# Optimization experiments

Hardware: AMD Instinct MI355X
Metric: run time of the kernel (lower is better)

The kernel has to match this reference:

```python
import jax, jax.numpy as jnp
import numpy as np

BS, DIM, HID, T = 4096, 64, 256, 101
GAMMA = 0.1
EPS = 1e-12  # pinverse guard for the 1x1 matrix G G^T


def setup_inputs() -> dict:
    key = jax.random.key(0)
    k0, k1, k2, k3 = jax.random.split(key, 4)
    return {
        "y0": jax.random.normal(k0, (BS, DIM), dtype=jnp.float32),
        "t": jnp.linspace(0.0, 1.0, T).astype(jnp.float32),
        "W1": jax.random.normal(k1, (DIM, HID), dtype=jnp.float32) * 0.05,
        "b1": jnp.zeros((HID,), dtype=jnp.float32),
        "W2": jax.random.normal(k2, (HID, DIM), dtype=jnp.float32) * 0.05,
        "b2": jnp.zeros((DIM,), dtype=jnp.float32),
        "wg": jax.random.normal(k3, (DIM,), dtype=jnp.float32) * 0.1,
        "bg": jnp.zeros((), dtype=jnp.float32),
    }


def reference(y0, t, W1, b1, W2, b2, wg, bg):
    # f_model: 2-layer tanh MLP (ignores t, as is common for autonomous dynamics)
    def f_model(ti, u):
        return jnp.tanh(u @ W1 + b1) @ W2 + b2  # (bs, dim)

    # g_fn: scalar constraint per sample
    def g_single(ui):
        return jnp.tanh(ui @ wg + bg)  # scalar

    def dynamic(ti, u):
        f_u = f_model(ti, u)                              # (bs, dim)
        g_u = jax.vmap(g_single)(u)                       # (bs,)
        # Torch detaches u before autograd Jacobian (create_graph keeps param path)
        G = jax.vmap(jax.grad(g_single))(jax.lax.stop_gradient(u))  # (bs, dim) == G_u row
        # F_u = G^T (G G^T)^+ ; G G^T is 1x1 -> scalar pinverse
        s = jnp.sum(G * G, axis=-1)                       # (bs,)
        pinv = jnp.where(jnp.abs(s) > EPS, 1.0 / s, 0.0)  # (bs,)
        stable = GAMMA * (g_u * pinv)[:, None] * G        # (bs, dim)
        return f_u - stable

    dt = t[1] - t[0]  # Euler solver uses constant dt

    def step(y, ti):
        y_new = y + dynamic(ti, y) * dt
        return y_new, y_new

    _, ys = jax.lax.scan(step, y0, t[:-1])
    return jnp.concatenate([y0[None], ys], axis=0)  # (T, bs, dim)
```

## Files before the change

kernel.cpp:

```cpp
#include <hip/hip_runtime.h>


#define GAMMA 0.1f
#define EPSG  1e-12f

typedef __attribute__((ext_vector_type(8))) short bf16x8;
typedef __attribute__((ext_vector_type(4))) float f32x4;

__device__ __forceinline__ float ftanh(float x) {
    float e = __expf(2.0f * x);
    return 1.0f - 2.0f * __builtin_amdgcn_rcpf(e + 1.0f);
}

__device__ __forceinline__ unsigned int f2bf(float f) {
    unsigned int u = __float_as_uint(f);
    return (u + 0x7fffu + ((u >> 16) & 1u)) >> 16;
}

__global__ __launch_bounds__(512, 1) void snde_kernel(
    const float* __restrict__ y0, const float* __restrict__ t,
    const float* __restrict__ W1, const float* __restrict__ b1,
    const float* __restrict__ W2, const float* __restrict__ b2,
    const float* __restrict__ wg, const float* __restrict__ bgp,
    float* __restrict__ out)
{
    __shared__ unsigned short uAs[16 * 64];
    __shared__ unsigned short hAs[16 * 256];
    __shared__ float          fpart[8][16][68];

    const int tid = threadIdx.x;
    const int w   = tid >> 6;
    const int l   = tid & 63;
    const int l15 = l & 15;
    const int lg  = l >> 4;
    const int s0g = blockIdx.x * 16;

    bf16x8 B1[2][2];
    #pragma unroll
    for (int nt = 0; nt < 2; ++nt) {
        const int n = w * 32 + nt * 16 + l15;
        #pragma unroll
        for (int kt = 0; kt < 2; ++kt) {
            bf16x8 v;
            #pragma unroll
            for (int j = 0; j < 8; ++j) {
                const int k = kt * 32 + lg * 8 + j;
                v[j] = (short)f2bf(W1[k * 256 + n]);
            }
            B1[nt][kt] = v;
        }
    }
    bf16x8 B2[4];
    #pragma unroll
    for (int nt = 0; nt < 4; ++nt) {
        const int n = nt * 16 + l15;
        bf16x8 v;
        #pragma unroll
        for (int j = 0; j < 8; ++j) {
            const int k = w * 32 + lg * 8 + j;
            v[j] = (short)f2bf(W2[k * 64 + n]);
        }
        B2[nt] = v;
    }

    float b1v[2];
    #pragma unroll
    for (int nt = 0; nt < 2; ++nt) b1v[nt] = b1[w * 32 + nt * 16 + l15];

    const int sU = tid >> 5;
    const int dd = (tid & 31) * 2;
    const float2 wg2  = *(const float2*)(&wg[dd]);
    const float2 b2v2 = *(const float2*)(&b2[dd]);
    float wsum = wg2.x * wg2.x + wg2.y * wg2.y;
    #pragma unroll
    for (int m = 1; m < 32; m <<= 1) wsum += __shfl_xor(wsum, m, 64);
    const float bg  = bgp[0];
    const float dtv = t[1] - t[0];

    float2 uv;
    {
        uv = *(const float2*)(&y0[(size_t)(s0g + sU) * 64 + dd]);
        unsigned int p0 = f2bf(uv.x) | (f2bf(uv.y) << 16);
        unsigned int off = (((unsigned)(sU * 128 + dd * 2)) ^ ((unsigned)(sU & 7) << 4)) >> 2;
        ((unsigned int*)uAs)[off] = p0;
        *(float2*)(&out[(size_t)(s0g + sU) * 64 + dd]) = uv;
    }
    __syncthreads();

    for (int step = 0; step < 100; ++step) {
        bf16x8 A1[2];
        #pragma unroll
        for (int kt = 0; kt < 2; ++kt) {
            unsigned int boff = ((unsigned)(l15 * 128 + (kt * 32 + lg * 8) * 2))
                              ^ ((unsigned)(l15 & 7) << 4);
            A1[kt] = *(const bf16x8*)((const char*)uAs + boff);
        }
        f32x4 acc1[2];
        #pragma unroll
        for (int nt = 0; nt < 2; ++nt) {
            acc1[nt][0] = b1v[nt]; acc1[nt][1] = b1v[nt];
            acc1[nt][2] = b1v[nt]; acc1[nt][3] = b1v[nt];
        }
        #pragma unroll
        for (int nt = 0; nt < 2; ++nt)
            #pragma unroll
            for (int kt = 0; kt < 2; ++kt)
                acc1[nt] = __builtin_amdgcn_mfma_f32_16x16x32_bf16(A1[kt], B1[nt][kt], acc1[nt], 0, 0, 0);

        #pragma unroll
        for (int nt = 0; nt < 2; ++nt) {
            const int n = w * 32 + nt * 16 + l15;
            #pragma unroll
            for (int i = 0; i < 4; ++i) {
                const int m = lg * 4 + i;
                const float th = ftanh(acc1[nt][i]);
                unsigned int boff = ((unsigned)(m * 512 + n * 2)) ^ ((unsigned)(m & 7) << 4);
                *(unsigned short*)((char*)hAs + boff) = (unsigned short)f2bf(th);
            }
        }

        bf16x8 A2;
        {
            unsigned int boff = ((unsigned)(l15 * 512 + (w * 32 + lg * 8) * 2))
                              ^ ((unsigned)(l15 & 7) << 4);
            A2 = *(const bf16x8*)((const char*)hAs + boff);
        }
        f32x4 acc2[4];
        #pragma unroll
        for (int nt = 0; nt < 4; ++nt) {
            acc2[nt][0] = 0.f; acc2[nt][1] = 0.f; acc2[nt][2] = 0.f; acc2[nt][3] = 0.f;
        }
        #pragma unroll
        for (int nt = 0; nt < 4; ++nt)
            acc2[nt] = __builtin_amdgcn_mfma_f32_16x16x32_bf16(A2, B2[nt], acc2[nt], 0, 0, 0);

        #pragma unroll
        for (int nt = 0; nt < 4; ++nt) {
            const int n = nt * 16 + l15;
            #pragma unroll
            for (int i = 0; i < 4; ++i)
                fpart[w][lg * 4 + i][n] = acc2[nt][i];
        }
        __syncthreads();

        {
            float2 fs = {0.f, 0.f};
            #pragma unroll
            for (int p = 0; p < 8; ++p) {
                const float2 fp = *(const float2*)(&fpart[p][sU][dd]);
                fs.x += fp.x; fs.y += fp.y;
            }
            float zp = uv.x * wg2.x + uv.y * wg2.y;
            #pragma unroll
            for (int m = 1; m < 32; m <<= 1) zp += __shfl_xor(zp, m, 64);
            const float th = ftanh(zp + bg);
            const float q  = 1.0f - th * th;
            const float sg = q * q * wsum;
            const float pinv = (fabsf(sg) > EPSG) ? __builtin_amdgcn_rcpf(sg) : 0.0f;
            const float coef = GAMMA * th * pinv * q;
            float2 un;
            un.x = uv.x + (fs.x + b2v2.x - coef * wg2.x) * dtv;
            un.y = uv.y + (fs.y + b2v2.y - coef * wg2.y) * dtv;
            uv = un;
            unsigned int p0 = f2bf(un.x) | (f2bf(un.y) << 16);
            unsigned int off = (((unsigned)(sU * 128 + dd * 2)) ^ ((unsigned)(sU & 7) << 4)) >> 2;
            ((unsigned int*)uAs)[off] = p0;
            *(float2*)(&out[(size_t)(step + 1) * (4096 * 64) + (size_t)(s0g + sU) * 64 + dd]) = un;
        }
        __syncthreads();
    }
}

extern "C" void kernel_launch(void* const* d_in, const int* in_sizes, int n_in,
                              void* d_out, int out_size, void* d_ws, size_t ws_size,
                              hipStream_t stream) {
    const float* y0 = (const float*)d_in[0];
    const float* t  = (const float*)d_in[1];
    const float* W1 = (const float*)d_in[2];
    const float* b1 = (const float*)d_in[3];
    const float* W2 = (const float*)d_in[4];
    const float* b2 = (const float*)d_in[5];
    const float* wg = (const float*)d_in[6];
    const float* bg = (const float*)d_in[7];
    float* out = (float*)d_out;

    snde_kernel<<<dim3(256), dim3(512), 0, stream>>>(y0, t, W1, b1, W2, b2, wg, bg, out);
}
```

Before: 111.2 us.

## Halve samples per block to launch 512 blocks and raise occupancy bound

Each block now handles 8 samples instead of 16, and the grid grows from 256 to 512 blocks so every CU on the device gets work. The MFMA tiles stay 16 rows wide with the unused rows zero-filled, so half of the matrix work in each block is padding. Each wave now owns one sample, so the per-sample reduction spans 64 lanes. The launch bound is raised to allow several blocks per CU. This spreads the sequential 100-step loop across more CUs and hides barrier latency, at the cost of wasted MFMA work and scalar instead of float2 stores.

```diff
diff --git a/kernel.cpp b/kernel.cpp
--- a/kernel.cpp
+++ b/kernel.cpp
@@ -17,7 +17,7 @@
     return (u + 0x7fffu + ((u >> 16) & 1u)) >> 16;
 }
 
-__global__ __launch_bounds__(512, 1) void snde_kernel(
+__global__ __launch_bounds__(512, 4) void snde_kernel(
     const float* __restrict__ y0, const float* __restrict__ t,
     const float* __restrict__ W1, const float* __restrict__ b1,
     const float* __restrict__ W2, const float* __restrict__ b2,
@@ -33,7 +33,7 @@
     const int l   = tid & 63;
     const int l15 = l & 15;
     const int lg  = l >> 4;
-    const int s0g = blockIdx.x * 16;
+    const int s0g = blockIdx.x * 8;
 
     bf16x8 B1[2][2];
     #pragma unroll
@@ -67,23 +67,23 @@
     #pragma unroll
     for (int nt = 0; nt < 2; ++nt) b1v[nt] = b1[w * 32 + nt * 16 + l15];
 
-    const int sU = tid >> 5;
-    const int dd = (tid & 31) * 2;
-    const float2 wg2  = *(const float2*)(&wg[dd]);
-    const float2 b2v2 = *(const float2*)(&b2[dd]);
-    float wsum = wg2.x * wg2.x + wg2.y * wg2.y;
+    const int sU = w;
+    const int dd = l;
+    const float wgv  = wg[dd];
+    const float b2v  = b2[dd];
+    float wsum = wgv * wgv;
     #pragma unroll
-    for (int m = 1; m < 32; m <<= 1) wsum += __shfl_xor(wsum, m, 64);
+    for (int m = 1; m < 64; m <<= 1) wsum += __shfl_xor(wsum, m, 64);
     const float bg  = bgp[0];
     const float dtv = t[1] - t[0];
 
-    float2 uv;
+    ((unsigned int*)uAs)[tid] = 0u;
+    __syncthreads();
+    float uv = y0[(size_t)(s0g + sU) * 64 + dd];
     {
-        uv = *(const float2*)(&y0[(size_t)(s0g + sU) * 64 + dd]);
-        unsigned int p0 = f2bf(uv.x) | (f2bf(uv.y) << 16);
-        unsigned int off = (((unsigned)(sU * 128 + dd * 2)) ^ ((unsigned)(sU & 7) << 4)) >> 2;
-        ((unsigned int*)uAs)[off] = p0;
-        *(float2*)(&out[(size_t)(s0g + sU) * 64 + dd]) = uv;
+        unsigned int boff = ((unsigned)(sU * 128 + dd * 2)) ^ ((unsigned)(sU & 7) << 4);
+        *(unsigned short*)((char*)uAs + boff) = (unsigned short)f2bf(uv);
+        out[(size_t)(s0g + sU) * 64 + dd] = uv;
     }
     __syncthreads();
 
@@ -144,28 +144,22 @@
         __syncthreads();
 
         {
-            float2 fs = {0.f, 0.f};
+            float fs = 0.f;
             #pragma unroll
-            for (int p = 0; p < 8; ++p) {
-                const float2 fp = *(const float2*)(&fpart[p][sU][dd]);
-                fs.x += fp.x; fs.y += fp.y;
-            }
-            float zp = uv.x * wg2.x + uv.y * wg2.y;
+            for (int p = 0; p < 8; ++p) fs += fpart[p][sU][dd];
+            float zp = uv * wgv;
             #pragma unroll
-            for (int m = 1; m < 32; m <<= 1) zp += __shfl_xor(zp, m, 64);
+            for (int m = 1; m < 64; m <<= 1) zp += __shfl_xor(zp, m, 64);
             const float th = ftanh(zp + bg);
             const float q  = 1.0f - th * th;
             const float sg = q * q * wsum;
             const float pinv = (fabsf(sg) > EPSG) ? __builtin_amdgcn_rcpf(sg) : 0.0f;
             const float coef = GAMMA * th * pinv * q;
-            float2 un;
-            un.x = uv.x + (fs.x + b2v2.x - coef * wg2.x) * dtv;
-            un.y = uv.y + (fs.y + b2v2.y - coef * wg2.y) * dtv;
+            const float un = uv + (fs + b2v - coef * wgv) * dtv;
             uv = un;
-            unsigned int p0 = f2bf(un.x) | (f2bf(un.y) << 16);
-            unsigned int off = (((unsigned)(sU * 128 + dd * 2)) ^ ((unsigned)(sU & 7) << 4)) >> 2;
-            ((unsigned int*)uAs)[off] = p0;
-            *(float2*)(&out[(size_t)(step + 1) * (4096 * 64) + (size_t)(s0g + sU) * 64 + dd]) = un;
+            unsigned int boff = ((unsigned)(sU * 128 + dd * 2)) ^ ((unsigned)(sU & 7) << 4);
+            *(unsigned short*)((char*)uAs + boff) = (unsigned short)f2bf(un);
+            out[(size_t)(step + 1) * (4096 * 64) + (size_t)(s0g + sU) * 64 + dd] = un;
         }
         __syncthreads();
     }
@@ -184,5 +178,5 @@
     const float* bg = (const float*)d_in[7];
     float* out = (float*)d_out;
 
-    snde_kernel<<<dim3(256), dim3(512), 0, stream>>>(y0, t, W1, b1, W2, b2, wg, bg, out);
+    snde_kernel<<<dim3(512), dim3(512), 0, stream>>>(y0, t, W1, b1, W2, b2, wg, bg, out);
 }
```

New measurement: 152.4 us. +37.0%, slower.
